# Performance work log

Hardware: AMD Instinct MI355X
Metric: run time of the kernel (lower is better)

## Reference

```python
import jax, jax.numpy as jnp
import numpy as np

D_MODEL = 1024
N_HEADS = 16
D_K = D_MODEL // N_HEADS
NEG = -1e9


def setup_inputs() -> dict:
    key = jax.random.key(0)
    ks = jax.random.split(key, 10)
    B, S = 4, 2048
    x = jax.random.normal(ks[0], (B, S, D_MODEL), dtype=jnp.float32)
    mask = jax.random.randint(ks[1], (B, S, S), 0, 2).astype(jnp.bool_)
    sc = 1.0 / np.sqrt(D_MODEL)
    Wq = jax.random.normal(ks[2], (D_MODEL, D_MODEL), dtype=jnp.float32) * sc
    bq = jnp.zeros((D_MODEL,), dtype=jnp.float32)
    Wk = jax.random.normal(ks[3], (D_MODEL, D_MODEL), dtype=jnp.float32) * sc
    bk = jnp.zeros((D_MODEL,), dtype=jnp.float32)
    Wv = jax.random.normal(ks[4], (D_MODEL, D_MODEL), dtype=jnp.float32) * sc
    bv = jnp.zeros((D_MODEL,), dtype=jnp.float32)
    Wo = jax.random.normal(ks[5], (D_MODEL, D_MODEL), dtype=jnp.float32) * sc
    bo = jnp.zeros((D_MODEL,), dtype=jnp.float32)
    return {"x": x, "mask": mask, "Wq": Wq, "bq": bq, "Wk": Wk, "bk": bk,
            "Wv": Wv, "bv": bv, "Wo": Wo, "bo": bo}


def _split_heads(t, B, S):
    # [B,S,d_model] -> [B,H,S,d_k]
    return t.reshape(B, S, N_HEADS, D_K).transpose(0, 2, 1, 3)


def reference(x, mask, Wq, bq, Wk, bk, Wv, bv, Wo, bo):
    B, S, _ = x.shape
    Q = _split_heads(x @ Wq + bq, B, S)
    K = _split_heads(x @ Wk + bk, B, S)
    V = _split_heads(x @ Wv + bv, B, S)
    scale = jnp.sqrt(jnp.float32(D_K))
    scores = jnp.einsum('bhqd,bhkd->bhqk', Q, K) / scale
    scores = jnp.where(mask[:, None, :, :], jnp.float32(NEG), scores)
    attn = jax.nn.softmax(scores, axis=-1)
    ctx = jnp.einsum('bhqk,bhkd->bhqd', attn, V)
    ctx = ctx.transpose(0, 2, 1, 3).reshape(B, S, D_MODEL)
    return ctx @ Wo + bo
```

## Files before the change

### kernel.cpp

```cpp
#include <hip/hip_runtime.h>

#define D_MODEL 1024
#define N_HEADS 16
#define D_K     64
#define BATCH   4
#define SEQ     2048
#define MROWS   (BATCH * SEQ)
#define QSCALE  0.18033688011112042f

typedef __bf16 bf16x8 __attribute__((ext_vector_type(8)));
typedef float  f32x4  __attribute__((ext_vector_type(4)));
typedef float  f32x16 __attribute__((ext_vector_type(16)));
typedef unsigned short ushort8 __attribute__((ext_vector_type(8)));
typedef unsigned short ushort4v __attribute__((ext_vector_type(4)));

#if __has_builtin(__builtin_amdgcn_exp2f)
#define EXP2F(x) __builtin_amdgcn_exp2f(x)
#else
#define EXP2F(x) exp2f(x)
#endif

#define CVT_PK_BF16(d, a, b) \
    asm("v_cvt_pk_bf16_f32 %0, %1, %2" : "=v"(d) : "v"(a), "v"(b))
#define PERMSWAP(a, b) \
    asm("v_permlane32_swap_b32 %0, %1" : "+v"(a), "+v"(b))

__device__ inline unsigned short f2bf(float f) {
    union { float f; unsigned int u; } v; v.f = f;
    unsigned int u = v.u;
    unsigned int r = (u + 0x7fffu + ((u >> 16) & 1u)) >> 16;
    return (unsigned short)r;
}

__device__ inline void load_lds16(const void* g, void* l) {
    __builtin_amdgcn_global_load_lds(
        (const __attribute__((address_space(1))) unsigned int*)g,
        (__attribute__((address_space(3))) unsigned int*)l, 16, 0, 0);
}

__global__ __launch_bounds__(256) void wprep(const float* __restrict__ Wq,
                                             const float* __restrict__ Wk,
                                             const float* __restrict__ Wv,
                                             const float* __restrict__ Wo,
                                             unsigned short* __restrict__ wt) {
    __shared__ __align__(16) unsigned short t[64][65];
    int w  = blockIdx.z;
    const float* W = (w == 0) ? Wq : (w == 1) ? Wk : (w == 2) ? Wv : Wo;
    int k0 = blockIdx.x * 64, n0 = blockIdx.y * 64;
    int tid = threadIdx.x;
    int nl = tid & 63, kq = tid >> 6;
#pragma unroll
    for (int i = 0; i < 16; i++) {
        int kl = kq * 16 + i;
        t[kl][nl] = f2bf(W[(size_t)(k0 + kl) * D_MODEL + n0 + nl]);
    }
    __syncthreads();
    unsigned short* out = wt + (size_t)w * D_MODEL * D_MODEL;
#pragma unroll
    for (int p = 0; p < 2; p++) {
        int nrow = p * 32 + (tid >> 3);
        int c8   = (tid & 7) * 8;
        ushort8 o;
#pragma unroll
        for (int j = 0; j < 8; j++) o[j] = t[c8 + j][nrow];
        *reinterpret_cast<ushort8*>(out + (size_t)(n0 + nrow) * D_MODEL + k0 + c8) = o;
    }
}

__global__ __launch_bounds__(256) void xprep(const float4* __restrict__ x,
                                             unsigned short* __restrict__ xb) {
    int i = blockIdx.x * 256 + threadIdx.x;
    float4 v = x[i];
    ushort4v o;
    o[0] = f2bf(v.x); o[1] = f2bf(v.y); o[2] = f2bf(v.z); o[3] = f2bf(v.w);
    *reinterpret_cast<ushort4v*>(xb + (size_t)i * 4) = o;
}

__global__ __launch_bounds__(256) void mprep(const int* __restrict__ mask,
                                             unsigned long long* __restrict__ mb) {
    int row = blockIdx.x;
    int tid = threadIdx.x;
    int wv  = tid >> 6;
#pragma unroll
    for (int w = 0; w < 8; w++) {
        int col = w * 256 + tid;
        int mval = mask[(size_t)row * SEQ + col];
        unsigned long long bits = __ballot(mval != 0);
        if ((tid & 63) == 0) mb[(size_t)row * 32 + w * 4 + wv] = bits;
    }
}

__global__ __launch_bounds__(256) void qkv_gemm(const unsigned short* __restrict__ xb,
                                                const unsigned short* __restrict__ wt,
                                                const float* __restrict__ bq,
                                                const float* __restrict__ bk,
                                                const float* __restrict__ bvv,
                                                unsigned short* __restrict__ qb,
                                                unsigned short* __restrict__ kb,
                                                unsigned short* __restrict__ vt) {
    __shared__ __align__(16) unsigned short lds_a[128 * 32];
    __shared__ __align__(16) unsigned short lds_b[128 * 32];
    int tid = threadIdx.x;
    int wave = tid >> 6, lane = tid & 63;
    int c = lane & 15, g = lane >> 4;
    int wave_m = (wave & 1) * 64, wave_n = (wave >> 1) * 64;
    int nblk = blockIdx.x * 128, mblk = blockIdx.y * 128;

    int oct0 = wave * 128 + lane, oct1 = oct0 + 64;
    int ra0 = oct0 >> 2, ga0 = ((oct0 & 3) ^ (ra0 & 3)) * 8;
    int ra1 = oct1 >> 2, ga1 = ((oct1 & 3) ^ (ra1 & 3)) * 8;
    const unsigned short* pa0 = xb + (size_t)(mblk + ra0) * D_MODEL + ga0;
    const unsigned short* pa1 = xb + (size_t)(mblk + ra1) * D_MODEL + ga1;
    const unsigned short* pb0 = wt + (size_t)(nblk + ra0) * D_MODEL + ga0;
    const unsigned short* pb1 = wt + (size_t)(nblk + ra1) * D_MODEL + ga1;
    unsigned short* la0 = lds_a + wave * 1024;
    unsigned short* la1 = la0 + 512;
    unsigned short* lb0 = lds_b + wave * 1024;
    unsigned short* lb1 = lb0 + 512;

    int aoff[4], boff[4];
#pragma unroll
    for (int mi = 0; mi < 4; mi++) {
        int row = wave_m + mi * 16 + c;
        aoff[mi] = (row * 4 + (g ^ (row & 3))) * 16;
    }
#pragma unroll
    for (int ni = 0; ni < 4; ni++) {
        int row = wave_n + ni * 16 + c;
        boff[ni] = (row * 4 + (g ^ (row & 3))) * 16;
    }

    f32x4 acc[4][4];
#pragma unroll
    for (int mi = 0; mi < 4; mi++)
#pragma unroll
        for (int ni = 0; ni < 4; ni++) acc[mi][ni] = f32x4{0.f, 0.f, 0.f, 0.f};

    for (int k0 = 0; k0 < D_MODEL; k0 += 32) {
        load_lds16(pa0 + k0, la0);
        load_lds16(pa1 + k0, la1);
        load_lds16(pb0 + k0, lb0);
        load_lds16(pb1 + k0, lb1);
        __syncthreads();
        bf16x8 af[4], bfr[4];
#pragma unroll
        for (int mi = 0; mi < 4; mi++)
            af[mi] = *reinterpret_cast<const bf16x8*>(reinterpret_cast<const char*>(lds_a) + aoff[mi]);
#pragma unroll
        for (int ni = 0; ni < 4; ni++)
            bfr[ni] = *reinterpret_cast<const bf16x8*>(reinterpret_cast<const char*>(lds_b) + boff[ni]);
#pragma unroll
        for (int mi = 0; mi < 4; mi++)
#pragma unroll
            for (int ni = 0; ni < 4; ni++)
                acc[mi][ni] = __builtin_amdgcn_mfma_f32_16x16x32_bf16(af[mi], bfr[ni], acc[mi][ni], 0, 0, 0);
        __syncthreads();
    }

    int nb = nblk + wave_n;
    int wsel = nb >> 10;
    int h = (nb >> 6) & 15;
    int dk0 = nb & 63;
    int mglob = mblk + wave_m;
    int b = mglob >> 11;
    int s0 = mglob & (SEQ - 1);
    size_t bh = (size_t)(b * N_HEADS + h);
    const float* bias = (wsel == 0) ? bq : (wsel == 1) ? bk : bvv;
    int nn = nb & (D_MODEL - 1);
    float bval[4];
#pragma unroll
    for (int ni = 0; ni < 4; ni++) bval[ni] = bias[nn + ni * 16 + c];
    float oscale = (wsel == 0) ? QSCALE : 1.0f;

    if (wsel < 2) {
        unsigned short* outp = wsel ? kb : qb;
#pragma unroll
        for (int mi = 0; mi < 4; mi++)
#pragma unroll
            for (int ni = 0; ni < 4; ni++) {
                int dk = dk0 + ni * 16 + c;
#pragma unroll
                for (int r = 0; r < 4; r++) {
                    int s = s0 + mi * 16 + g * 4 + r;
                    outp[(bh * SEQ + s) * 64 + dk] = f2bf((acc[mi][ni][r] + bval[ni]) * oscale);
                }
            }
    } else {
#pragma unroll
        for (int mi = 0; mi < 4; mi++)
#pragma unroll
            for (int ni = 0; ni < 4; ni++) {
                int dk = dk0 + ni * 16 + c;
                int s = s0 + mi * 16 + g * 4;
                ushort4v o;
#pragma unroll
                for (int r = 0; r < 4; r++) o[r] = f2bf(acc[mi][ni][r] + bval[ni]);
                *reinterpret_cast<ushort4v*>(vt + (bh * 64 + dk) * SEQ + s) = o;
            }
    }
}

__global__ __launch_bounds__(128, 2) void attn(const unsigned short* __restrict__ qb,
                                               const unsigned short* __restrict__ kb,
                                               const unsigned short* __restrict__ vt,
                                               const unsigned long long* __restrict__ mb,
                                               unsigned short* __restrict__ ctx) {
    __shared__ __align__(16) unsigned char smem[16384];
    unsigned short* lk = (unsigned short*)smem;
    unsigned short* lv = (unsigned short*)(smem + 8192);

    int tid = threadIdx.x;
    int wave = tid >> 6, lane = tid & 63;
    int q31 = lane & 31, hi = lane >> 5;
    int bh = blockIdx.x >> 4;
    int q0 = (blockIdx.x & 15) * 128 + wave * 64;
    int b = bh >> 4, h = bh & 15;
    const unsigned short* qbase = qb + (size_t)bh * SEQ * 64;
    const unsigned short* kbase = kb + (size_t)bh * SEQ * 64;
    const unsigned short* vbase = vt + (size_t)bh * 64 * SEQ;
    const unsigned long long* mp0 = mb + ((size_t)b * SEQ + q0 + q31) * 32;
    const unsigned long long* mp1 = mp0 + 1024;

    bf16x8 qf[2][4];
#pragma unroll
    for (int t = 0; t < 2; t++) {
        const unsigned short* qr = qbase + (size_t)(q0 + 32 * t + q31) * 64 + hi * 8;
#pragma unroll
        for (int c = 0; c < 4; c++)
            qf[t][c] = *reinterpret_cast<const bf16x8*>(qr + c * 16);
    }

    int srow = lane >> 3;
    int soct = (lane & 7) ^ srow;
    const unsigned short* ksrc[4];
    const unsigned short* vsrc[4];
    unsigned short* klb[4];
    unsigned short* vlb[4];
#pragma unroll
    for (int i = 0; i < 4; i++) {
        int rbase = 16 * i + 8 * wave;
        ksrc[i] = kbase + (size_t)(rbase + srow) * 64 + soct * 8;
        vsrc[i] = vbase + (size_t)(rbase + srow) * SEQ + soct * 8;
        klb[i] = lk + rbase * 64;
        vlb[i] = lv + rbase * 64;
    }

    int kofs[2][4];
#pragma unroll
    for (int s = 0; s < 2; s++)
#pragma unroll
        for (int c = 0; c < 4; c++)
            kofs[s][c] = (32 * s + q31) * 128 + (((hi + 2 * c) ^ (q31 & 7)) * 16);

    float lsum[2] = {0.f, 0.f};
    f32x16 po[2][2];
#pragma unroll
    for (int i = 0; i < 16; i++) {
        po[0][0][i] = 0.f; po[0][1][i] = 0.f;
        po[1][0][i] = 0.f; po[1][1][i] = 0.f;
    }

    for (int it = 0; it < SEQ / 64; it++) {
#pragma unroll
        for (int i = 0; i < 4; i++) {
            load_lds16(ksrc[i] + it * 4096, klb[i]);
            load_lds16(vsrc[i] + it * 64, vlb[i]);
        }
        unsigned long long w64[2];
        w64[0] = mp0[it];
        w64[1] = mp1[it];
        __syncthreads();

        const char* lkb = (const char*)lk;
        const char* lvb = (const char*)lv;

#pragma unroll
        for (int s = 0; s < 2; s++) {
            f32x16 sq[2];
#pragma unroll
            for (int i = 0; i < 16; i++) { sq[0][i] = 0.f; sq[1][i] = 0.f; }
#pragma unroll
            for (int c = 0; c < 4; c++) {
                bf16x8 kf = *reinterpret_cast<const bf16x8*>(lkb + kofs[s][c]);
                sq[0] = __builtin_amdgcn_mfma_f32_32x32x16_bf16(kf, qf[0][c], sq[0], 0, 0, 0);
                sq[1] = __builtin_amdgcn_mfma_f32_32x32x16_bf16(kf, qf[1][c], sq[1], 0, 0, 0);
            }
            union PF { uint4 u; bf16x8 v; };
            PF pf[2][2];
#pragma unroll
            for (int t = 0; t < 2; t++) {
                unsigned int wt_ = ~(unsigned int)(w64[t] >> (32 * s));
                float pm[16];
#pragma unroll
                for (int j = 0; j < 4; j++) {
                    unsigned int nj = wt_ >> (8 * j + 4 * hi);
#pragma unroll
                    for (int e = 0; e < 4; e++) {
                        float p = EXP2F(sq[t][4 * j + e]);
                        unsigned int m = (unsigned int)((int)(nj << (31 - e)) >> 31);
                        unsigned int pu = __float_as_uint(p) & m;
                        pm[4 * j + e] = __uint_as_float(pu);
                        lsum[t] += __uint_as_float(pu);
                    }
                }
                unsigned int w[8];
#pragma unroll
                for (int j = 0; j < 4; j++) {
                    CVT_PK_BF16(w[2 * j],     pm[4 * j + 0], pm[4 * j + 1]);
                    CVT_PK_BF16(w[2 * j + 1], pm[4 * j + 2], pm[4 * j + 3]);
                }
                PERMSWAP(w[0], w[2]); PERMSWAP(w[1], w[3]);
                PERMSWAP(w[4], w[6]); PERMSWAP(w[5], w[7]);
                pf[t][0].u = uint4{w[0], w[1], w[2], w[3]};
                pf[t][1].u = uint4{w[4], w[5], w[6], w[7]};
            }
#pragma unroll
            for (int cp = 0; cp < 2; cp++) {
                int c = 2 * s + cp;
#pragma unroll
                for (int so = 0; so < 2; so++) {
                    bf16x8 vf = *reinterpret_cast<const bf16x8*>(lvb + kofs[so][c]);
                    po[0][so] = __builtin_amdgcn_mfma_f32_32x32x16_bf16(vf, pf[0][cp].v, po[0][so], 0, 0, 0);
                    po[1][so] = __builtin_amdgcn_mfma_f32_32x32x16_bf16(vf, pf[1][cp].v, po[1][so], 0, 0, 0);
                }
            }
        }
        __syncthreads();
    }

    float inv[2];
#pragma unroll
    for (int t = 0; t < 2; t++) {
        lsum[t] += __shfl_xor(lsum[t], 32);
        inv[t] = 1.f / lsum[t];
    }

    unsigned int* ob = (unsigned int*)(smem + wave * 8192);
    int csw = 4 * (q31 & 7);
#pragma unroll
    for (int t = 0; t < 2; t++) {
        unsigned int* obr = ob + (32 * t + q31) * 32;
#pragma unroll
        for (int so = 0; so < 2; so++)
#pragma unroll
            for (int j = 0; j < 4; j++) {
                unsigned int w0 = (unsigned int)f2bf(po[t][so][4 * j + 0] * inv[t])
                                | ((unsigned int)f2bf(po[t][so][4 * j + 1] * inv[t]) << 16);
                unsigned int w1 = (unsigned int)f2bf(po[t][so][4 * j + 2] * inv[t])
                                | ((unsigned int)f2bf(po[t][so][4 * j + 3] * inv[t]) << 16);
                int d = (16 * so + 4 * j + 2 * hi) ^ csw;
                uint2 u; u.x = w0; u.y = w1;
                *reinterpret_cast<uint2*>(obr + d) = u;
            }
    }
    __builtin_amdgcn_s_waitcnt(0);
    size_t crow = (size_t)b * SEQ + q0;
    int o = lane & 7, rl = lane >> 3;
#pragma unroll
    for (int i = 0; i < 8; i++) {
        int r = 8 * i + rl;
        uint4 v = *reinterpret_cast<const uint4*>(ob + r * 32 + 4 * (o ^ (r & 7)));
        *reinterpret_cast<uint4*>(ctx + (crow + r) * D_MODEL + h * 64 + o * 8) = v;
    }
}

__global__ __launch_bounds__(256) void oproj(const unsigned short* __restrict__ ctx,
                                             const unsigned short* __restrict__ wt,
                                             const float* __restrict__ bo,
                                             float* __restrict__ out) {
    __shared__ __align__(16) unsigned short lds_a[128 * 32];
    __shared__ __align__(16) unsigned short lds_b[128 * 32];
    int tid = threadIdx.x;
    int wave = tid >> 6, lane = tid & 63;
    int c = lane & 15, g = lane >> 4;
    int wave_m = (wave & 1) * 64, wave_n = (wave >> 1) * 64;
    int nblk = blockIdx.x * 128, mblk = blockIdx.y * 128;
    const unsigned short* wo = wt + (size_t)3 * D_MODEL * D_MODEL;

    int oct0 = wave * 128 + lane, oct1 = oct0 + 64;
    int ra0 = oct0 >> 2, ga0 = ((oct0 & 3) ^ (ra0 & 3)) * 8;
    int ra1 = oct1 >> 2, ga1 = ((oct1 & 3) ^ (ra1 & 3)) * 8;
    const unsigned short* pa0 = ctx + (size_t)(mblk + ra0) * D_MODEL + ga0;
    const unsigned short* pa1 = ctx + (size_t)(mblk + ra1) * D_MODEL + ga1;
    const unsigned short* pb0 = wo + (size_t)(nblk + ra0) * D_MODEL + ga0;
    const unsigned short* pb1 = wo + (size_t)(nblk + ra1) * D_MODEL + ga1;
    unsigned short* la0 = lds_a + wave * 1024;
    unsigned short* la1 = la0 + 512;
    unsigned short* lb0 = lds_b + wave * 1024;
    unsigned short* lb1 = lb0 + 512;

    int aoff[4], boff[4];
#pragma unroll
    for (int mi = 0; mi < 4; mi++) {
        int row = wave_m + mi * 16 + c;
        aoff[mi] = (row * 4 + (g ^ (row & 3))) * 16;
    }
#pragma unroll
    for (int ni = 0; ni < 4; ni++) {
        int row = wave_n + ni * 16 + c;
        boff[ni] = (row * 4 + (g ^ (row & 3))) * 16;
    }

    f32x4 acc[4][4];
#pragma unroll
    for (int mi = 0; mi < 4; mi++)
#pragma unroll
        for (int ni = 0; ni < 4; ni++) acc[mi][ni] = f32x4{0.f, 0.f, 0.f, 0.f};

    for (int k0 = 0; k0 < D_MODEL; k0 += 32) {
        load_lds16(pa0 + k0, la0);
        load_lds16(pa1 + k0, la1);
        load_lds16(pb0 + k0, lb0);
        load_lds16(pb1 + k0, lb1);
        __syncthreads();
        bf16x8 af[4], bfr[4];
#pragma unroll
        for (int mi = 0; mi < 4; mi++)
            af[mi] = *reinterpret_cast<const bf16x8*>(reinterpret_cast<const char*>(lds_a) + aoff[mi]);
#pragma unroll
        for (int ni = 0; ni < 4; ni++)
            bfr[ni] = *reinterpret_cast<const bf16x8*>(reinterpret_cast<const char*>(lds_b) + boff[ni]);
#pragma unroll
        for (int mi = 0; mi < 4; mi++)
#pragma unroll
            for (int ni = 0; ni < 4; ni++)
                acc[mi][ni] = __builtin_amdgcn_mfma_f32_16x16x32_bf16(af[mi], bfr[ni], acc[mi][ni], 0, 0, 0);
        __syncthreads();
    }

    float bval[4];
#pragma unroll
    for (int ni = 0; ni < 4; ni++) bval[ni] = bo[nblk + wave_n + ni * 16 + c];
#pragma unroll
    for (int mi = 0; mi < 4; mi++)
#pragma unroll
        for (int ni = 0; ni < 4; ni++) {
            int n = nblk + wave_n + ni * 16 + c;
#pragma unroll
            for (int r = 0; r < 4; r++) {
                int m = mblk + wave_m + mi * 16 + g * 4 + r;
                out[(size_t)m * D_MODEL + n] = acc[mi][ni][r] + bval[ni];
            }
        }
}

extern "C" void kernel_launch(void* const* d_in, const int* in_sizes, int n_in,
                              void* d_out, int out_size, void* d_ws, size_t ws_size,
                              hipStream_t stream) {
    const float* x    = (const float*)d_in[0];
    const int*   mask = (const int*)d_in[1];
    const float* Wq = (const float*)d_in[2];
    const float* bq = (const float*)d_in[3];
    const float* Wk = (const float*)d_in[4];
    const float* bk = (const float*)d_in[5];
    const float* Wv = (const float*)d_in[6];
    const float* bv = (const float*)d_in[7];
    const float* Wo = (const float*)d_in[8];
    const float* bo = (const float*)d_in[9];
    float* out = (float*)d_out;

    char* ws = (char*)d_ws;
    const size_t MB = 1024 * 1024;
    unsigned short* wt  = (unsigned short*)(ws + 0 * MB);
    unsigned short* xb  = (unsigned short*)(ws + 8 * MB);
    unsigned short* qb  = (unsigned short*)(ws + 24 * MB);
    unsigned short* kb  = (unsigned short*)(ws + 40 * MB);
    unsigned short* vt  = (unsigned short*)(ws + 56 * MB);
    unsigned short* ctx = (unsigned short*)(ws + 72 * MB);
    unsigned long long* mb = (unsigned long long*)(ws + 88 * MB);

    wprep<<<dim3(16, 16, 4), 256, 0, stream>>>(Wq, Wk, Wv, Wo, wt);
    xprep<<<dim3(MROWS * D_MODEL / 4 / 256), 256, 0, stream>>>((const float4*)x, xb);
    mprep<<<dim3(MROWS), 256, 0, stream>>>(mask, mb);
    qkv_gemm<<<dim3(24, 64), 256, 0, stream>>>(xb, wt, bq, bk, bv, qb, kb, vt);
    attn<<<dim3(1024), 128, 0, stream>>>(qb, kb, vt, mb, ctx);
    oproj<<<dim3(8, 64), 256, 0, stream>>>(ctx, wt, bo, out);
}
```

Before: 389.9 us.

## Double-buffer K/V LDS tiles and prefetch mask words in attention loop

Doubles the attention kernel's LDS to two K/V stages. The next tile's async global-to-LDS loads and mask words are issued before computing on the current tile, with a partial vmcnt wait and raw s_barrier replacing __syncthreads. This is meant to hide global load latency behind the MFMA work. It doubles LDS use per block, which may limit occupancy, and it relies on hand-counted vmcnt values being correct.

```diff
diff --git a/kernel.cpp b/kernel.cpp
--- a/kernel.cpp
+++ b/kernel.cpp
@@ -24,6 +24,8 @@
     asm("v_cvt_pk_bf16_f32 %0, %1, %2" : "=v"(d) : "v"(a), "v"(b))
 #define PERMSWAP(a, b) \
     asm("v_permlane32_swap_b32 %0, %1" : "+v"(a), "+v"(b))
+#define WAIT_VM(N) asm volatile("s_waitcnt vmcnt(" #N ")" ::: "memory")
+#define CFENCE()   asm volatile("" ::: "memory")
 
 __device__ inline unsigned short f2bf(float f) {
     union { float f; unsigned int u; } v; v.f = f;
@@ -205,9 +207,7 @@
                                                const unsigned short* __restrict__ vt,
                                                const unsigned long long* __restrict__ mb,
                                                unsigned short* __restrict__ ctx) {
-    __shared__ __align__(16) unsigned char smem[16384];
-    unsigned short* lk = (unsigned short*)smem;
-    unsigned short* lv = (unsigned short*)(smem + 8192);
+    __shared__ __align__(16) unsigned char smem[32768];
 
     int tid = threadIdx.x;
     int wave = tid >> 6, lane = tid & 63;
@@ -234,15 +234,13 @@
     int soct = (lane & 7) ^ srow;
     const unsigned short* ksrc[4];
     const unsigned short* vsrc[4];
-    unsigned short* klb[4];
-    unsigned short* vlb[4];
+    int stg[4];
 #pragma unroll
     for (int i = 0; i < 4; i++) {
         int rbase = 16 * i + 8 * wave;
         ksrc[i] = kbase + (size_t)(rbase + srow) * 64 + soct * 8;
         vsrc[i] = vbase + (size_t)(rbase + srow) * SEQ + soct * 8;
-        klb[i] = lk + rbase * 64;
-        vlb[i] = lv + rbase * 64;
+        stg[i]  = rbase * 128;
     }
 
     int kofs[2][4];
@@ -260,19 +258,32 @@
         po[1][0][i] = 0.f; po[1][1][i] = 0.f;
     }
 
+    unsigned long long mnx0 = mp0[0], mnx1 = mp1[0];
+    CFENCE();
+#pragma unroll
+    for (int i = 0; i < 4; i++) {
+        load_lds16(ksrc[i], smem + stg[i]);
+        load_lds16(vsrc[i], smem + 8192 + stg[i]);
+    }
+
     for (int it = 0; it < SEQ / 64; it++) {
+        unsigned long long w64[2];
+        w64[0] = mnx0; w64[1] = mnx1;
+        int itn = (it + 1 < SEQ / 64) ? it + 1 : it;
+        mnx0 = mp0[itn]; mnx1 = mp1[itn];
+        CFENCE();
+        unsigned char* bufn = smem + ((it + 1) & 1) * 16384;
 #pragma unroll
         for (int i = 0; i < 4; i++) {
-            load_lds16(ksrc[i] + it * 4096, klb[i]);
-            load_lds16(vsrc[i] + it * 64, vlb[i]);
+            load_lds16(ksrc[i] + itn * 4096, bufn + stg[i]);
+            load_lds16(vsrc[i] + itn * 64,  bufn + 8192 + stg[i]);
         }
-        unsigned long long w64[2];
-        w64[0] = mp0[it];
-        w64[1] = mp1[it];
-        __syncthreads();
-
-        const char* lkb = (const char*)lk;
-        const char* lvb = (const char*)lv;
+        WAIT_VM(10);
+        __builtin_amdgcn_s_barrier();
+        CFENCE();
+
+        const char* lkb = (const char*)(smem + (it & 1) * 16384);
+        const char* lvb = lkb + 8192;
 
 #pragma unroll
         for (int s = 0; s < 2; s++) {
@@ -325,8 +336,12 @@
                 }
             }
         }
-        __syncthreads();
-    }
+        CFENCE();
+        __builtin_amdgcn_s_barrier();
+    }
+
+    WAIT_VM(0);
+    __builtin_amdgcn_s_barrier();
 
     float inv[2];
 #pragma unroll
```

Result: faster. 363.9 us (-6.7%).
